# Kernel tuning notes

Measured on AMD Instinct MI355X. Metric: run time of the kernel, lower is better.

## Reference

```python
import jax, jax.numpy as jnp
import numpy as np

B, C, E, TOPK = 8192, 1024, 8, 4
H = 4 * C  # mlp_ratio = 4.0
EPS = 1e-6


def quick_gelu(x):
    return x * jax.nn.sigmoid(1.702 * x)


def layer_norm(x, gamma, beta):
    mu = jnp.mean(x, axis=-1, keepdims=True)
    var = jnp.var(x, axis=-1, keepdims=True)
    return (x - mu) * jax.lax.rsqrt(var + EPS) * gamma + beta


def setup_inputs() -> dict:
    key = jax.random.key(0)
    ks = jax.random.split(key, 8)
    s1 = 1.0 / np.sqrt(C)
    s2 = 1.0 / np.sqrt(H)
    return {
        "x": jax.random.normal(ks[0], (B, C), dtype=jnp.float32),
        "W1": jax.random.uniform(ks[1], (E, C, H), jnp.float32, -s1, s1),
        "b1": jax.random.uniform(ks[2], (E, H), jnp.float32, -s1, s1),
        "W2": jax.random.uniform(ks[3], (E, H, C), jnp.float32, -s2, s2),
        "b2": jax.random.uniform(ks[4], (E, C), jnp.float32, -s2, s2),
        "ln_g": jnp.ones((E, C), jnp.float32),
        "ln_b": jnp.zeros((E, C), jnp.float32),
        "Wg": jax.random.uniform(ks[5], (C, E), jnp.float32, -s1, s1),
        "bg": jax.random.uniform(ks[6], (E,), jnp.float32, -s1, s1),
    }


def reference(x, W1, b1, W2, b2, ln_g, ln_b, Wg, bg):
    # gate + softmax + top-k
    scores = jax.nn.softmax(x @ Wg + bg, axis=-1)           # [B, E]
    topk_scores, topk_idx = jax.lax.top_k(scores, TOPK)     # [B, K]
    # all experts on all tokens (naive MoE, matches original)
    h = quick_gelu(jnp.einsum('bc,ech->beh', x, W1) + b1)   # [B, E, H]
    y = quick_gelu(jnp.einsum('beh,ehc->bec', h, W2) + b2)  # [B, E, C]
    y = layer_norm(y, ln_g, ln_b)                            # [B, E, C]
    # gather top-k expert outputs and weighted-combine
    topk_out = jnp.take_along_axis(y, topk_idx[:, :, None], axis=1)  # [B, K, C]
    return jnp.sum(topk_out * topk_scores[:, :, None], axis=1)       # [B, C]
```

## Files before the change

kernel.cpp:

```cpp
#include <hip/hip_runtime.h>

#define NB 8192
#define NC 1024
#define NE 8
#define NK 4
#define NH 4096
constexpr int ROWCAP = NB * NK + NE * 128;

typedef _Float16 f16;
typedef _Float16 f16x8 __attribute__((ext_vector_type(8)));
typedef _Float16 f16x4 __attribute__((ext_vector_type(4)));
typedef float    f32x4 __attribute__((ext_vector_type(4)));

__device__ __forceinline__ void async_cp16(const f16* g, f16* l) {
    __builtin_amdgcn_global_load_lds((const __attribute__((address_space(1))) void*)g,
                                     (__attribute__((address_space(3))) void*)l, 16, 0, 0);
}

__device__ __forceinline__ float quick_gelu(float v) {
    return v / (1.f + __expf(-1.702f * v));
}

__global__ void transpose_cast_k(const float* __restrict__ in, f16* __restrict__ out,
                                 int R, int S) {
    __shared__ f16 tile[32][33];
    int e = blockIdx.z;
    long base = (long)e * R * S;
    int s0 = blockIdx.x * 32, r0 = blockIdx.y * 32;
    int tx = threadIdx.x & 31, ty = threadIdx.x >> 5;
    #pragma unroll
    for (int i = 0; i < 32; i += 8)
        tile[ty + i][tx] = (f16)in[base + (long)(r0 + ty + i) * S + s0 + tx];
    __syncthreads();
    #pragma unroll
    for (int i = 0; i < 32; i += 8)
        out[base + (long)(s0 + ty + i) * R + r0 + tx] = tile[tx][ty + i];
}

__global__ void gating_k(const float* __restrict__ x, const float* __restrict__ Wg,
                         const float* __restrict__ bg, int* __restrict__ counts,
                         int* __restrict__ tokmap, int* __restrict__ eids,
                         int* __restrict__ slots, float* __restrict__ gatew,
                         f16* __restrict__ x16) {
    int b = blockIdx.x, t = threadIdx.x;
    float acc[NE] = {};
    float4 xv = ((const float4*)(x + (long)b * NC))[t];
    f16x4 hx = { (f16)xv.x, (f16)xv.y, (f16)xv.z, (f16)xv.w };
    ((f16x4*)(x16 + (long)b * NC))[t] = hx;
    const float* wr = Wg + (long)t * 4 * NE;
    #pragma unroll
    for (int j = 0; j < 4; j++) {
        float xj = ((const float*)&xv)[j];
        #pragma unroll
        for (int e2 = 0; e2 < NE; e2++) acc[e2] += xj * wr[j * NE + e2];
    }
    #pragma unroll
    for (int e2 = 0; e2 < NE; e2++)
        #pragma unroll
        for (int off = 32; off; off >>= 1) acc[e2] += __shfl_down(acc[e2], off);
    __shared__ float red[4][NE];
    int lane = t & 63, w = t >> 6;
    if (lane == 0)
        for (int e2 = 0; e2 < NE; e2++) red[w][e2] = acc[e2];
    __syncthreads();
    if (t == 0) {
        float l[NE];
        float m = -1e30f;
        for (int e2 = 0; e2 < NE; e2++) {
            l[e2] = red[0][e2] + red[1][e2] + red[2][e2] + red[3][e2] + bg[e2];
            m = fmaxf(m, l[e2]);
        }
        float p[NE], sum = 0.f;
        for (int e2 = 0; e2 < NE; e2++) { p[e2] = __expf(l[e2] - m); sum += p[e2]; }
        float inv = 1.f / sum;
        for (int e2 = 0; e2 < NE; e2++) p[e2] *= inv;
        bool taken[NE] = {};
        for (int k = 0; k < NK; k++) {
            int be = 0; float bv = -1e30f;
            for (int e2 = 0; e2 < NE; e2++)
                if (!taken[e2] && p[e2] > bv) { bv = p[e2]; be = e2; }
            taken[be] = true;
            int slot = atomicAdd(&counts[be], 1);
            tokmap[be * NB + slot] = b;
            eids[b * NK + k] = be;
            slots[b * NK + k] = slot;
            gatew[b * NK + k] = bv;
        }
    }
}

__global__ void offsets_k(const int* __restrict__ counts, int* __restrict__ offp) {
    if (threadIdx.x == 0 && blockIdx.x == 0) {
        int o = 0;
        for (int e = 0; e < NE; e++) { offp[e] = o; o += ((counts[e] + 127) >> 7) << 7; }
    }
}

__global__ __launch_bounds__(256) void gemm_f16(
    const f16* __restrict__ A, const f16* __restrict__ Bt,
    const float* __restrict__ bias, f16* __restrict__ Out,
    const int* __restrict__ counts, const int* __restrict__ offp,
    const int* __restrict__ tokmap, int Kd, int N, int gather) {
    int e = blockIdx.z;
    int cnt = counts[e];
    int m0 = blockIdx.x << 7;
    if (m0 >= cnt) return;
    int n0 = blockIdx.y << 7;
    int base = offp[e];

    __shared__ __align__(16) f16 At[128 * 32];
    __shared__ __align__(16) f16 Bs[128 * 32];

    int t = threadIdx.x;
    int lane = t & 63;
    int w = t >> 6;
    int wm = (w >> 1) << 6, wn = (w & 1) << 6;

    int sr = m0 + (t >> 2);
    int sc = (((t & 3) ^ ((t >> 3) & 3)) << 3);
    int ca = sr < cnt - 1 ? sr : cnt - 1;
    int cb = sr + 64 < cnt - 1 ? sr + 64 : cnt - 1;
    long arow0, arow1;
    if (gather) { arow0 = tokmap[e * NB + ca]; arow1 = tokmap[e * NB + cb]; }
    else        { arow0 = base + ca;           arow1 = base + cb; }
    const f16* ap0 = A + arow0 * (long)Kd + sc;
    const f16* ap1 = A + arow1 * (long)Kd + sc;
    const f16* bp0 = Bt + ((long)e * N + n0 + (t >> 2)) * (long)Kd + sc;
    const f16* bp1 = bp0 + (long)64 * Kd;

    f32x4 acc[4][4] = {};
    int ml = lane & 15;
    int sxq = (((lane >> 4) ^ ((ml >> 1) & 3)) << 3);
    const f16* ard[4];
    const f16* brd[4];
    #pragma unroll
    for (int mi = 0; mi < 4; mi++) ard[mi] = &At[(wm + mi * 16 + ml) * 32 + sxq];
    #pragma unroll
    for (int ni = 0; ni < 4; ni++) brd[ni] = &Bs[(wn + ni * 16 + ml) * 32 + sxq];
    f16* la0 = &At[t * 8];
    f16* la1 = &At[2048 + t * 8];
    f16* lb0 = &Bs[t * 8];
    f16* lb1 = &Bs[2048 + t * 8];

    for (int k0 = 0; k0 < Kd; k0 += 32) {
        async_cp16(ap0, la0); ap0 += 32;
        async_cp16(ap1, la1); ap1 += 32;
        async_cp16(bp0, lb0); bp0 += 32;
        async_cp16(bp1, lb1); bp1 += 32;
        __syncthreads();
        f16x8 af[4], bf[4];
        #pragma unroll
        for (int mi = 0; mi < 4; mi++) af[mi] = *(const f16x8*)ard[mi];
        #pragma unroll
        for (int ni = 0; ni < 4; ni++) bf[ni] = *(const f16x8*)brd[ni];
        #pragma unroll
        for (int mi = 0; mi < 4; mi++)
            #pragma unroll
            for (int ni = 0; ni < 4; ni++)
                acc[mi][ni] = __builtin_amdgcn_mfma_f32_16x16x32_f16(af[mi], bf[ni], acc[mi][ni], 0, 0, 0);
        __syncthreads();
    }

    int rq = (lane >> 4) << 2;
    #pragma unroll
    for (int ni = 0; ni < 4; ni++) {
        int col = n0 + wn + ni * 16 + ml;
        float bv = bias[(long)e * N + col];
        #pragma unroll
        for (int mi = 0; mi < 4; mi++) {
            int r0 = m0 + wm + mi * 16 + rq;
            #pragma unroll
            for (int rr = 0; rr < 4; rr++) {
                int row = r0 + rr;
                if (row < cnt) {
                    float v = acc[mi][ni][rr] + bv;
                    Out[(long)(base + row) * N + col] = (f16)quick_gelu(v);
                }
            }
        }
    }
}

__global__ void ln_combine_k(const f16* __restrict__ y16, const float* __restrict__ lng,
                             const float* __restrict__ lnb, const int* __restrict__ eids,
                             const int* __restrict__ slots, const float* __restrict__ gatew,
                             const int* __restrict__ offp, float* __restrict__ out) {
    int b = blockIdx.x, t = threadIdx.x;
    int lane = t & 63, w = t >> 6;
    __shared__ float red[4][2];
    float o[4] = {0.f, 0.f, 0.f, 0.f};
    int c0 = t * 4;
    for (int k = 0; k < NK; k++) {
        int e = eids[b * NK + k];
        long r = offp[e] + slots[b * NK + k];
        float wk = gatew[b * NK + k];
        f16x4 hv = *(const f16x4*)(y16 + r * NC + c0);
        float v[4];
        #pragma unroll
        for (int j = 0; j < 4; j++) v[j] = (float)hv[j];
        float s = v[0] + v[1] + v[2] + v[3];
        float ss = v[0] * v[0] + v[1] * v[1] + v[2] * v[2] + v[3] * v[3];
        #pragma unroll
        for (int off = 32; off; off >>= 1) { s += __shfl_down(s, off); ss += __shfl_down(ss, off); }
        if (lane == 0) { red[w][0] = s; red[w][1] = ss; }
        __syncthreads();
        float S  = red[0][0] + red[1][0] + red[2][0] + red[3][0];
        float SS = red[0][1] + red[1][1] + red[2][1] + red[3][1];
        float mu = S * (1.f / NC);
        float var = SS * (1.f / NC) - mu * mu;
        float rs = rsqrtf(var + 1e-6f);
        #pragma unroll
        for (int j = 0; j < 4; j++) {
            float g  = lng[(long)e * NC + c0 + j];
            float bb = lnb[(long)e * NC + c0 + j];
            o[j] += wk * ((v[j] - mu) * rs * g + bb);
        }
        __syncthreads();
    }
    float4 ov = {o[0], o[1], o[2], o[3]};
    ((float4*)(out + (long)b * NC))[t] = ov;
}

extern "C" void kernel_launch(void* const* d_in, const int* in_sizes, int n_in,
                              void* d_out, int out_size, void* d_ws, size_t ws_size,
                              hipStream_t stream) {
    const float* x   = (const float*)d_in[0];
    const float* W1  = (const float*)d_in[1];
    const float* b1  = (const float*)d_in[2];
    const float* W2  = (const float*)d_in[3];
    const float* b2  = (const float*)d_in[4];
    const float* lng = (const float*)d_in[5];
    const float* lnb = (const float*)d_in[6];
    const float* Wg  = (const float*)d_in[7];
    const float* bg  = (const float*)d_in[8];
    float* out = (float*)d_out;

    char* ws = (char*)d_ws;
    size_t o = 0;
    auto take = [&](size_t bytes) { char* p = ws + o; o += (bytes + 255) & ~(size_t)255; return p; };
    f16*   x16    = (f16*)take((size_t)NB * NC * 2);
    f16*   w1t    = (f16*)take((size_t)NE * NH * NC * 2);
    f16*   w2t    = (f16*)take((size_t)NE * NC * NH * 2);
    f16*   h16    = (f16*)take((size_t)ROWCAP * NH * 2);
    f16*   y16    = (f16*)take((size_t)ROWCAP * NC * 2);
    int*   tokmap = (int*)take((size_t)NE * NB * 4);
    int*   eids   = (int*)take((size_t)NB * NK * 4);
    int*   slots  = (int*)take((size_t)NB * NK * 4);
    float* gatew  = (float*)take((size_t)NB * NK * 4);
    int*   counts = (int*)take(256);
    int*   offp   = (int*)take(256);

    hipMemsetAsync(counts, 0, NE * sizeof(int), stream);
    transpose_cast_k<<<dim3(NH / 32, NC / 32, NE), 256, 0, stream>>>(W1, w1t, NC, NH);
    transpose_cast_k<<<dim3(NC / 32, NH / 32, NE), 256, 0, stream>>>(W2, w2t, NH, NC);
    gating_k<<<NB, 256, 0, stream>>>(x, Wg, bg, counts, tokmap, eids, slots, gatew, x16);
    offsets_k<<<1, 64, 0, stream>>>(counts, offp);
    gemm_f16<<<dim3(64, NH / 128, NE), 256, 0, stream>>>(x16, w1t, b1, h16, counts, offp, tokmap, NC, NH, 1);
    gemm_f16<<<dim3(64, NC / 128, NE), 256, 0, stream>>>(h16, w2t, b2, y16, counts, offp, tokmap, NH, NC, 0);
    ln_combine_k<<<NB, 256, 0, stream>>>(y16, lng, lnb, eids, slots, gatew, offp, out);
}
```

Measured before the change: 1.921 ms.

## Double-buffer GEMM LDS tiles and stage epilogue through LDS for vector stores

The GEMM main loop now uses two LDS buffers, so the async global-to-LDS copy for the next K-slice is issued before the MFMAs on the current one. This is meant to hide load latency and drop one barrier per iteration. The epilogue writes bias+GELU results into a padded LDS tile in two halves and then stores 16-byte vectors per row, replacing the scattered 2-byte global stores. LDS use doubles to 32KB, which may reduce occupancy, and the epilogue adds extra barriers.

```diff
diff --git a/kernel.cpp b/kernel.cpp
--- a/kernel.cpp
+++ b/kernel.cpp
@@ -108,8 +108,7 @@
     int n0 = blockIdx.y << 7;
     int base = offp[e];
 
-    __shared__ __align__(16) f16 At[128 * 32];
-    __shared__ __align__(16) f16 Bs[128 * 32];
+    __shared__ __align__(16) f16 smem[16384];
 
     int t = threadIdx.x;
     int lane = t & 63;
@@ -128,31 +127,32 @@
     const f16* bp0 = Bt + ((long)e * N + n0 + (t >> 2)) * (long)Kd + sc;
     const f16* bp1 = bp0 + (long)64 * Kd;
 
+    auto stage = [&](int q) {
+        f16* d = smem + (q << 13) + (t << 3);
+        async_cp16(ap0, d);        ap0 += 32;
+        async_cp16(ap1, d + 2048); ap1 += 32;
+        async_cp16(bp0, d + 4096); bp0 += 32;
+        async_cp16(bp1, d + 6144); bp1 += 32;
+    };
+
     f32x4 acc[4][4] = {};
     int ml = lane & 15;
     int sxq = (((lane >> 4) ^ ((ml >> 1) & 3)) << 3);
-    const f16* ard[4];
-    const f16* brd[4];
-    #pragma unroll
-    for (int mi = 0; mi < 4; mi++) ard[mi] = &At[(wm + mi * 16 + ml) * 32 + sxq];
-    #pragma unroll
-    for (int ni = 0; ni < 4; ni++) brd[ni] = &Bs[(wn + ni * 16 + ml) * 32 + sxq];
-    f16* la0 = &At[t * 8];
-    f16* la1 = &At[2048 + t * 8];
-    f16* lb0 = &Bs[t * 8];
-    f16* lb1 = &Bs[2048 + t * 8];
-
-    for (int k0 = 0; k0 < Kd; k0 += 32) {
-        async_cp16(ap0, la0); ap0 += 32;
-        async_cp16(ap1, la1); ap1 += 32;
-        async_cp16(bp0, lb0); bp0 += 32;
-        async_cp16(bp1, lb1); bp1 += 32;
-        __syncthreads();
+    int aoff = (wm + ml) * 32 + sxq;
+    int boff = (wn + ml) * 32 + sxq + 4096;
+
+    int nIter = Kd >> 5;
+    stage(0);
+    __syncthreads();
+    for (int it = 0; it < nIter; ++it) {
+        int p = it & 1;
+        if (it + 1 < nIter) stage(p ^ 1);
+        const f16* sb = smem + (p << 13);
         f16x8 af[4], bf[4];
         #pragma unroll
-        for (int mi = 0; mi < 4; mi++) af[mi] = *(const f16x8*)ard[mi];
-        #pragma unroll
-        for (int ni = 0; ni < 4; ni++) bf[ni] = *(const f16x8*)brd[ni];
+        for (int mi = 0; mi < 4; mi++) af[mi] = *(const f16x8*)(sb + aoff + mi * 512);
+        #pragma unroll
+        for (int ni = 0; ni < 4; ni++) bf[ni] = *(const f16x8*)(sb + boff + ni * 512);
         #pragma unroll
         for (int mi = 0; mi < 4; mi++)
             #pragma unroll
@@ -161,23 +161,37 @@
         __syncthreads();
     }
 
+    const int EP = 136;
     int rq = (lane >> 4) << 2;
     #pragma unroll
-    for (int ni = 0; ni < 4; ni++) {
-        int col = n0 + wn + ni * 16 + ml;
-        float bv = bias[(long)e * N + col];
-        #pragma unroll
-        for (int mi = 0; mi < 4; mi++) {
-            int r0 = m0 + wm + mi * 16 + rq;
+    for (int h = 0; h < 2; ++h) {
+        if (wm == h * 64) {
             #pragma unroll
-            for (int rr = 0; rr < 4; rr++) {
-                int row = r0 + rr;
-                if (row < cnt) {
-                    float v = acc[mi][ni][rr] + bv;
-                    Out[(long)(base + row) * N + col] = (f16)quick_gelu(v);
+            for (int ni = 0; ni < 4; ni++) {
+                int col = wn + ni * 16 + ml;
+                float bv = bias[(long)e * N + n0 + col];
+                #pragma unroll
+                for (int mi = 0; mi < 4; mi++) {
+                    #pragma unroll
+                    for (int rr = 0; rr < 4; rr++) {
+                        int lr = mi * 16 + rq + rr;
+                        smem[lr * EP + col] = (f16)quick_gelu(acc[mi][ni][rr] + bv);
+                    }
                 }
             }
         }
+        __syncthreads();
+        int r = t >> 2;
+        int grow = m0 + h * 64 + r;
+        if (grow < cnt) {
+            long gbase = (long)(base + grow) * N + n0;
+            #pragma unroll
+            for (int j = 0; j < 4; j++) {
+                int cc = ((t & 3) + 4 * j) << 3;
+                *(f16x8*)(Out + gbase + cc) = *(const f16x8*)&smem[r * EP + cc];
+            }
+        }
+        __syncthreads();
     }
 }
 
```

After: 1.863 ms. 1.03x faster.
